# Kernel tuning notes

Hardware: AMD Instinct MI355X
Metric: run time of the kernel (lower is better)

Reference implementation:

```python
import jax, jax.numpy as jnp
import numpy as np

NUM_HEADS = 12

def setup_inputs() -> dict:
    key = jax.random.key(0)
    k1, k2, k3 = jax.random.split(key, 3)
    B, N, C = 8, 1024, 768
    x = jax.random.normal(k1, (B, N, C), dtype=jnp.float32)
    w_qkv = jax.random.normal(k2, (3 * C, C), dtype=jnp.float32) * (C ** -0.5)
    w_proj = jax.random.normal(k3, (C, C), dtype=jnp.float32) * (C ** -0.5)
    b_proj = jnp.zeros((C,), dtype=jnp.float32)
    return {"x": x, "w_qkv": w_qkv, "w_proj": w_proj, "b_proj": b_proj}

def reference(x, w_qkv, w_proj, b_proj):
    B, N, C = x.shape
    H = NUM_HEADS
    D = C // H
    scale = D ** -0.5
    # qkv projection: [B, N, 3C] -> [3, B, H, N, D]
    qkv = (x @ w_qkv.T).reshape(B, N, 3, H, D).transpose(2, 0, 3, 1, 4)
    q, k, v = qkv[0], qkv[1], qkv[2]
    # full N x N attention scores (unfused, as in the original module)
    attn = jnp.einsum("bhnd,bhmd->bhnm", q, k) * scale
    attn = jax.nn.softmax(attn, axis=-1)
    # attn_drop is identity at eval (p=0.0)
    out = jnp.einsum("bhnm,bhmd->bhnd", attn, v)  # [B, H, N, D]
    out = out.transpose(0, 2, 1, 3).reshape(B, N, C)
    out = out @ w_proj.T + b_proj
    # proj_drop identity at eval
    return (out, attn)
```

## Files before the change

### kernel.cpp

```cpp
#include <hip/hip_runtime.h>

#define Bb 8
#define Nn 1024
#define Cc 768
#define Hh 12
#define Dd 64
#define BHn (Bb*Hh)
#define Mm (Bb*Nn)
#define TCc (3*Cc)

typedef __bf16 bf16x8 __attribute__((ext_vector_type(8)));
typedef float  f32x4  __attribute__((ext_vector_type(4)));
typedef __attribute__((address_space(1))) const void* gas_ptr;
typedef __attribute__((address_space(3))) void* las_ptr;
typedef unsigned short u16;

__device__ __forceinline__ u16 bf16_rne(float f) {
    unsigned int u = __builtin_bit_cast(unsigned int, f);
    u += 0x7fffu + ((u >> 16) & 1u);
    return (u16)(u >> 16);
}
__device__ __forceinline__ void split_bf16(float f, u16& h, u16& l) {
    u16 hh = bf16_rne(f);
    float hf = __builtin_bit_cast(float, (unsigned int)hh << 16);
    h = hh;
    l = bf16_rne(f - hf);
}

__global__ __launch_bounds__(256)
void split_kernel(const float* __restrict__ src, u16* __restrict__ dh,
                  u16* __restrict__ dl, int n4)
{
    int stride = gridDim.x * blockDim.x;
    for (int i = blockIdx.x * blockDim.x + threadIdx.x; i < n4; i += stride) {
        float4 v = reinterpret_cast<const float4*>(src)[i];
        ushort4 h, l;
        split_bf16(v.x, h.x, l.x);
        split_bf16(v.y, h.y, l.y);
        split_bf16(v.z, h.z, l.z);
        split_bf16(v.w, h.w, l.w);
        reinterpret_cast<ushort4*>(dh)[i] = h;
        reinterpret_cast<ushort4*>(dl)[i] = l;
    }
}

__device__ __forceinline__ void gemm128_bf16x3(
    const u16* __restrict__ Agh, const u16* __restrict__ Agl,
    const u16* __restrict__ Bgh, const u16* __restrict__ Bgl,
    int m0, int j0, f32x4 acc[4][4])
{
    __shared__ __align__(16) u16 Ash[128*32];
    __shared__ __align__(16) u16 Asl[128*32];
    __shared__ __align__(16) u16 Bsh[128*32];
    __shared__ __align__(16) u16 Bsl[128*32];

    const int tid = threadIdx.x;
    const int ln = tid & 63, wid = tid >> 6;
    const int wr = wid >> 1, wc = wid & 1;

    const u16* gsrc =
        (wid == 0) ? Agh + (size_t)m0 * Cc :
        (wid == 1) ? Agl + (size_t)m0 * Cc :
        (wid == 2) ? Bgh + (size_t)j0 * Cc :
                     Bgl + (size_t)j0 * Cc;
    u16* lds = (wid == 0) ? Ash : (wid == 1) ? Asl : (wid == 2) ? Bsh : Bsl;

    const int lrow = ln >> 2, lslot = ln & 3;
    const int r16 = ln & 15,  ko = ln >> 4;

    f32x4 z = {0.f, 0.f, 0.f, 0.f};
#pragma unroll
    for (int mi = 0; mi < 4; ++mi)
#pragma unroll
        for (int ni = 0; ni < 4; ++ni) acc[mi][ni] = z;

    for (int k0 = 0; k0 < Cc; k0 += 32) {
#pragma unroll
        for (int c = 0; c < 8; ++c) {
            int row = c * 16 + lrow;
            int ss = lslot ^ ((row >> 1) & 3);
            const u16* gp = gsrc + (size_t)row * Cc + k0 + ss * 8;
            __builtin_amdgcn_global_load_lds((gas_ptr)gp, (las_ptr)(lds + c * 512), 16u, 0, 0);
        }
        __syncthreads();

        bf16x8 ah[4], al[4], bh[4], bl[4];
#pragma unroll
        for (int mi = 0; mi < 4; ++mi) {
            int row = wr*64 + mi*16 + r16;
            int ss = (ko ^ ((row >> 1) & 3)) * 8;
            ah[mi] = *reinterpret_cast<const bf16x8*>(Ash + row*32 + ss);
            al[mi] = *reinterpret_cast<const bf16x8*>(Asl + row*32 + ss);
        }
#pragma unroll
        for (int ni = 0; ni < 4; ++ni) {
            int row = wc*64 + ni*16 + r16;
            int ss = (ko ^ ((row >> 1) & 3)) * 8;
            bh[ni] = *reinterpret_cast<const bf16x8*>(Bsh + row*32 + ss);
            bl[ni] = *reinterpret_cast<const bf16x8*>(Bsl + row*32 + ss);
        }
#pragma unroll
        for (int mi = 0; mi < 4; ++mi)
#pragma unroll
            for (int ni = 0; ni < 4; ++ni) {
                acc[mi][ni] = __builtin_amdgcn_mfma_f32_16x16x32_bf16(ah[mi], bh[ni], acc[mi][ni], 0, 0, 0);
                acc[mi][ni] = __builtin_amdgcn_mfma_f32_16x16x32_bf16(ah[mi], bl[ni], acc[mi][ni], 0, 0, 0);
                acc[mi][ni] = __builtin_amdgcn_mfma_f32_16x16x32_bf16(al[mi], bh[ni], acc[mi][ni], 0, 0, 0);
            }
        __syncthreads();
    }
}

__global__ __launch_bounds__(256, 2)
void qkv_mfma(const u16* __restrict__ xh, const u16* __restrict__ xl,
              const u16* __restrict__ wh, const u16* __restrict__ wl,
              u16* __restrict__ Qh, u16* __restrict__ Ql,
              u16* __restrict__ Kh, u16* __restrict__ Kl,
              u16* __restrict__ Vth, u16* __restrict__ Vtl)
{
    const int m0 = blockIdx.x * 128, j0 = blockIdx.y * 128;
    f32x4 acc[4][4];
    gemm128_bf16x3(xh, xl, wh, wl, m0, j0, acc);

    const int tid = threadIdx.x;
    const int ln = tid & 63, wid = tid >> 6;
    const int wr = wid >> 1, wc = wid & 1;
    const int t3 = j0 / Cc;
    const int jr0 = j0 - t3 * Cc;

    if (t3 == 2) {
#pragma unroll
        for (int mi = 0; mi < 4; ++mi) {
            int gm0 = m0 + wr*64 + mi*16 + (ln >> 4) * 4;
            int b = gm0 >> 10, n0 = gm0 & 1023;
#pragma unroll
            for (int ni = 0; ni < 4; ++ni) {
                int col = jr0 + wc*64 + ni*16 + (ln & 15);
                int h = col >> 6, d = col & 63;
                u16 hh[4], ll[4];
#pragma unroll
                for (int i = 0; i < 4; ++i) split_bf16(acc[mi][ni][i], hh[i], ll[i]);
                size_t base = ((size_t)((b*Hh + h) * Dd + d)) * Nn + n0;
                *reinterpret_cast<ushort4*>(Vth + base) = make_ushort4(hh[0], hh[1], hh[2], hh[3]);
                *reinterpret_cast<ushort4*>(Vtl + base) = make_ushort4(ll[0], ll[1], ll[2], ll[3]);
            }
        }
    } else {
        u16* dh = (t3 == 0) ? Qh : Kh;
        u16* dl = (t3 == 0) ? Ql : Kl;
#pragma unroll
        for (int mi = 0; mi < 4; ++mi) {
            int gm0 = m0 + wr*64 + mi*16 + (ln >> 4) * 4;
            int b = gm0 >> 10, n0 = gm0 & 1023;
#pragma unroll
            for (int ni = 0; ni < 4; ++ni) {
                int col = jr0 + wc*64 + ni*16 + (ln & 15);
                int h = col >> 6, d = col & 63;
#pragma unroll
                for (int i = 0; i < 4; ++i) {
                    u16 hh, ll;
                    split_bf16(acc[mi][ni][i], hh, ll);
                    size_t base = ((size_t)((b*Hh + h) * Nn + n0 + i)) * Dd + d;
                    dh[base] = hh; dl[base] = ll;
                }
            }
        }
    }
}

__global__ __launch_bounds__(256, 2)
void scores_mfma(const u16* __restrict__ Qh_, const u16* __restrict__ Ql_,
                 const u16* __restrict__ Kh_, const u16* __restrict__ Kl_,
                 float* __restrict__ E, float* __restrict__ rowsum)
{
    __shared__ __align__(16) u16 sQh[128*64];
    __shared__ __align__(16) u16 sQl[128*64];
    __shared__ __align__(16) u16 sKh[128*64];
    __shared__ __align__(16) u16 sKl[128*64];

    const int tid = threadIdx.x;
    const int ln = tid & 63, wid = tid >> 6;
    const int wr = wid >> 1, wc = wid & 1;
    const int bh = blockIdx.z;
    const int i0 = blockIdx.x * 128, j0 = blockIdx.y * 128;
    const int r16 = ln & 15, ko = ln >> 4;

    {
        const u16* gsrc =
            (wid == 0) ? Qh_ + (size_t)(bh*Nn + i0) * Dd :
            (wid == 1) ? Ql_ + (size_t)(bh*Nn + i0) * Dd :
            (wid == 2) ? Kh_ + (size_t)(bh*Nn + j0) * Dd :
                         Kl_ + (size_t)(bh*Nn + j0) * Dd;
        u16* lds = (wid == 0) ? sQh : (wid == 1) ? sQl : (wid == 2) ? sKh : sKl;
        int r = ln >> 3, s = ln & 7;
        int ss = s ^ (r & 7);
        const u16* gp = gsrc + r*64 + ss*8;
#pragma unroll
        for (int c = 0; c < 16; ++c)
            __builtin_amdgcn_global_load_lds((gas_ptr)(gp + c*512), (las_ptr)(lds + c*512), 16u, 0, 0);
    }
    __syncthreads();

    f32x4 acc[4][4];
    f32x4 z = {0.f, 0.f, 0.f, 0.f};
#pragma unroll
    for (int mi = 0; mi < 4; ++mi)
#pragma unroll
        for (int ni = 0; ni < 4; ++ni) acc[mi][ni] = z;

#pragma unroll
    for (int kk = 0; kk < 2; ++kk) {
        bf16x8 qh[4], ql[4], kh[4], kl[4];
#pragma unroll
        for (int mi = 0; mi < 4; ++mi) {
            int row = wr*64 + mi*16 + r16;
            int s = (kk*4 + ko) ^ (row & 7);
            qh[mi] = *reinterpret_cast<const bf16x8*>(sQh + row*64 + s*8);
            ql[mi] = *reinterpret_cast<const bf16x8*>(sQl + row*64 + s*8);
        }
#pragma unroll
        for (int ni = 0; ni < 4; ++ni) {
            int row = wc*64 + ni*16 + r16;
            int s = (kk*4 + ko) ^ (row & 7);
            kh[ni] = *reinterpret_cast<const bf16x8*>(sKh + row*64 + s*8);
            kl[ni] = *reinterpret_cast<const bf16x8*>(sKl + row*64 + s*8);
        }
#pragma unroll
        for (int mi = 0; mi < 4; ++mi)
#pragma unroll
            for (int ni = 0; ni < 4; ++ni) {
                acc[mi][ni] = __builtin_amdgcn_mfma_f32_16x16x32_bf16(qh[mi], kh[ni], acc[mi][ni], 0, 0, 0);
                acc[mi][ni] = __builtin_amdgcn_mfma_f32_16x16x32_bf16(qh[mi], kl[ni], acc[mi][ni], 0, 0, 0);
                acc[mi][ni] = __builtin_amdgcn_mfma_f32_16x16x32_bf16(ql[mi], kh[ni], acc[mi][ni], 0, 0, 0);
            }
    }

    const float scale = 0.125f;
    float* Eb = E + (size_t)bh * Nn * Nn;
    float vsum[4][4];
#pragma unroll
    for (int mi = 0; mi < 4; ++mi)
#pragma unroll
        for (int i = 0; i < 4; ++i) vsum[mi][i] = 0.f;

#pragma unroll
    for (int mi = 0; mi < 4; ++mi) {
        int row = i0 + wr*64 + mi*16 + ko*4;
#pragma unroll
        for (int ni = 0; ni < 4; ++ni) {
            int col = j0 + wc*64 + ni*16 + r16;
#pragma unroll
            for (int i = 0; i < 4; ++i) {
                float v = __expf(acc[mi][ni][i] * scale);
                vsum[mi][i] += v;
                Eb[(size_t)(row + i) * Nn + col] = v;
            }
        }
    }
#pragma unroll
    for (int mi = 0; mi < 4; ++mi)
#pragma unroll
        for (int i = 0; i < 4; ++i) {
            float v = vsum[mi][i];
            v += __shfl_xor(v, 1); v += __shfl_xor(v, 2);
            v += __shfl_xor(v, 4); v += __shfl_xor(v, 8);
            vsum[mi][i] = v;
        }
    {
        int mi = r16 >> 2, i = r16 & 3;
        int row = i0 + wr*64 + mi*16 + ko*4 + i;
        atomicAdd(&rowsum[bh * Nn + row], vsum[mi][i]);
    }
}

__global__ __launch_bounds__(256, 2)
void pv_mfma(float* __restrict__ E, const u16* __restrict__ Vth, const u16* __restrict__ Vtl,
             const float* __restrict__ rowsum,
             u16* __restrict__ Oh, u16* __restrict__ Ol)
{
    __shared__ __align__(16) u16 sPh[128*64];
    __shared__ __align__(16) u16 sPl[128*64];
    __shared__ __align__(16) u16 sVh[64*64];
    __shared__ __align__(16) u16 sVl[64*64];
    __shared__ float inv_s[128];

    const int tid = threadIdx.x;
    const int ln = tid & 63, wid = tid >> 6;
    const int i0 = blockIdx.x * 128;
    const int bh = blockIdx.y;
    const int r16 = ln & 15, ko = ln >> 4;
    float* Eb = E + (size_t)bh * Nn * Nn;

    if (tid < 128) inv_s[tid] = 1.0f / rowsum[bh * Nn + i0 + tid];
    __syncthreads();

    f32x4 acc[2][4];
    f32x4 z = {0.f, 0.f, 0.f, 0.f};
#pragma unroll
    for (int mi = 0; mi < 2; ++mi)
#pragma unroll
        for (int ni = 0; ni < 4; ++ni) acc[mi][ni] = z;

    for (int j0 = 0; j0 < Nn; j0 += 64) {
        if (wid < 2) {
            const u16* gsrc = ((wid == 0) ? Vth : Vtl) + (size_t)bh * Dd * Nn + j0;
            u16* lds = (wid == 0) ? sVh : sVl;
            int r = ln >> 3, s = ln & 7;
            int ss = s ^ (r & 7);
            const u16* gp = gsrc + (size_t)r * Nn + ss*8;
#pragma unroll
            for (int c = 0; c < 8; ++c)
                __builtin_amdgcn_global_load_lds((gas_ptr)(gp + (size_t)c*8*Nn), (las_ptr)(lds + c*512), 16u, 0, 0);
        }
#pragma unroll
        for (int it = 0; it < 8; ++it) {
            int idx = tid + it * 256;
            int row = idx >> 4, c4 = idx & 15;
            float* gp = Eb + (size_t)(i0 + row) * Nn + j0 + c4*4;
            float4 e = *reinterpret_cast<const float4*>(gp);
            float is = inv_s[row];
            float4 p = make_float4(e.x*is, e.y*is, e.z*is, e.w*is);
            *reinterpret_cast<float4*>(gp) = p;
            u16 h[4], l[4];
            split_bf16(p.x, h[0], l[0]); split_bf16(p.y, h[1], l[1]);
            split_bf16(p.z, h[2], l[2]); split_bf16(p.w, h[3], l[3]);
            int s = (c4 >> 1) ^ (row & 7);
            int off = row*64 + s*8 + (c4 & 1)*4;
            *reinterpret_cast<ushort4*>(sPh + off) = make_ushort4(h[0], h[1], h[2], h[3]);
            *reinterpret_cast<ushort4*>(sPl + off) = make_ushort4(l[0], l[1], l[2], l[3]);
        }
        __syncthreads();

#pragma unroll
        for (int kk = 0; kk < 2; ++kk) {
            bf16x8 ph[2], pl[2], vh[4], vl[4];
#pragma unroll
            for (int mi = 0; mi < 2; ++mi) {
                int row = wid*32 + mi*16 + r16;
                int s = (kk*4 + ko) ^ (row & 7);
                ph[mi] = *reinterpret_cast<const bf16x8*>(sPh + row*64 + s*8);
                pl[mi] = *reinterpret_cast<const bf16x8*>(sPl + row*64 + s*8);
            }
#pragma unroll
            for (int ni = 0; ni < 4; ++ni) {
                int row = ni*16 + r16;
                int s = (kk*4 + ko) ^ (row & 7);
                vh[ni] = *reinterpret_cast<const bf16x8*>(sVh + row*64 + s*8);
                vl[ni] = *reinterpret_cast<const bf16x8*>(sVl + row*64 + s*8);
            }
#pragma unroll
            for (int mi = 0; mi < 2; ++mi)
#pragma unroll
                for (int ni = 0; ni < 4; ++ni) {
                    acc[mi][ni] = __builtin_amdgcn_mfma_f32_16x16x32_bf16(ph[mi], vh[ni], acc[mi][ni], 0, 0, 0);
                    acc[mi][ni] = __builtin_amdgcn_mfma_f32_16x16x32_bf16(ph[mi], vl[ni], acc[mi][ni], 0, 0, 0);
                    acc[mi][ni] = __builtin_amdgcn_mfma_f32_16x16x32_bf16(pl[mi], vh[ni], acc[mi][ni], 0, 0, 0);
                }
        }
        __syncthreads();
    }

    const int b = bh / Hh, h = bh % Hh;
#pragma unroll
    for (int mi = 0; mi < 2; ++mi) {
        int n0 = i0 + wid*32 + mi*16 + ko*4;
#pragma unroll
        for (int ni = 0; ni < 4; ++ni) {
            int d = ni*16 + r16;
#pragma unroll
            for (int i = 0; i < 4; ++i) {
                u16 hh, ll;
                split_bf16(acc[mi][ni][i], hh, ll);
                size_t base = ((size_t)(b * Nn + n0 + i)) * Cc + h * Dd + d;
                Oh[base] = hh; Ol[base] = ll;
            }
        }
    }
}

__global__ __launch_bounds__(256, 2)
void proj_mfma(const u16* __restrict__ oh, const u16* __restrict__ ol,
               const u16* __restrict__ wh, const u16* __restrict__ wl,
               const float* __restrict__ bias, float* __restrict__ out)
{
    const int m0 = blockIdx.x * 128, j0 = blockIdx.y * 128;
    f32x4 acc[4][4];
    gemm128_bf16x3(oh, ol, wh, wl, m0, j0, acc);

    const int tid = threadIdx.x;
    const int ln = tid & 63, wid = tid >> 6;
    const int wr = wid >> 1, wc = wid & 1;
#pragma unroll
    for (int mi = 0; mi < 4; ++mi) {
        int gm0 = m0 + wr*64 + mi*16 + (ln >> 4) * 4;
#pragma unroll
        for (int ni = 0; ni < 4; ++ni) {
            int col = j0 + wc*64 + ni*16 + (ln & 15);
            float bv = bias[col];
#pragma unroll
            for (int i = 0; i < 4; ++i)
                out[(size_t)(gm0 + i) * Cc + col] = acc[mi][ni][i] + bv;
        }
    }
}

extern "C" void kernel_launch(void* const* d_in, const int* in_sizes, int n_in,
                              void* d_out, int out_size, void* d_ws, size_t ws_size,
                              hipStream_t stream)
{
    const float* x      = (const float*)d_in[0];
    const float* w_qkv  = (const float*)d_in[1];
    const float* w_proj = (const float*)d_in[2];
    const float* b_proj = (const float*)d_in[3];

    float* out  = (float*)d_out;
    float* attn = out + (size_t)Mm * Cc;

    const size_t qkv_elems = (size_t)BHn * Nn * Dd;
    u16* Qh  = (u16*)d_ws;
    u16* Ql  = Qh  + qkv_elems;
    u16* Kh  = Ql  + qkv_elems;
    u16* Kl  = Kh  + qkv_elems;
    u16* Vth = Kl  + qkv_elems;
    u16* Vtl = Vth + qkv_elems;
    float* Oslot  = (float*)(Vtl + qkv_elems);
    float* rowsum = Oslot + (size_t)Mm * Cc;
    u16* wph = (u16*)(rowsum + (size_t)BHn * Nn);
    u16* wpl = wph + (size_t)Cc * Cc;

    u16* Oh = (u16*)Oslot;
    u16* Ol = Oh + (size_t)Mm * Cc;

    u16* xh  = (u16*)attn;
    u16* xl  = xh + (size_t)Mm * Cc;
    u16* wqh = xl + (size_t)Mm * Cc;
    u16* wql = wqh + (size_t)TCc * Cc;

    hipMemsetAsync(rowsum, 0, (size_t)BHn * Nn * sizeof(float), stream);

    split_kernel<<<dim3(2048), 256, 0, stream>>>(x,      xh,  xl,  (int)((size_t)Mm * Cc / 4));
    split_kernel<<<dim3(1728), 256, 0, stream>>>(w_qkv,  wqh, wql, (int)((size_t)TCc * Cc / 4));
    split_kernel<<<dim3(576),  256, 0, stream>>>(w_proj, wph, wpl, (int)((size_t)Cc * Cc / 4));

    qkv_mfma   <<<dim3(Mm/128, TCc/128), 256, 0, stream>>>(xh, xl, wqh, wql,
                                                           Qh, Ql, Kh, Kl, Vth, Vtl);
    scores_mfma<<<dim3(Nn/128, Nn/128, BHn), 256, 0, stream>>>(Qh, Ql, Kh, Kl, attn, rowsum);
    pv_mfma    <<<dim3(Nn/128, BHn), 256, 0, stream>>>(attn, Vth, Vtl, rowsum, Oh, Ol);
    proj_mfma  <<<dim3(Mm/128, Cc/128), 256, 0, stream>>>(Oh, Ol, wph, wpl, b_proj, out);
}
```

Before: 855.9 us.

## Fuse scores and PV into two-pass attention kernel with pre-swizzled Q/K layout

Replaces the separate scores and PV kernels with one fused attention kernel. A first pass recomputes QK^T to accumulate row sums of exp. A second pass recomputes the scores, writes normalized probabilities once, and feeds them straight into the PV MFMAs. This removes the unnormalized score write plus the read-modify-write of the full attention matrix, along with the atomic rowsum and the memset. In exchange, QK^T is computed twice. The QKV GEMM epilogue now stages Q/K through LDS and writes them in an XOR-swizzled tile image, so the fused kernel can load them with contiguous direct-to-LDS loads. Blocks are also remapped for locality.

```diff
diff --git a/kernel.cpp b/kernel.cpp
--- a/kernel.cpp
+++ b/kernel.cpp
@@ -25,6 +25,10 @@
     float hf = __builtin_bit_cast(float, (unsigned int)hh << 16);
     h = hh;
     l = bf16_rne(f - hf);
+}
+
+__device__ __forceinline__ int img_off(int row, int d) {
+    return row*64 + (((d >> 3) ^ (row & 7)) << 3) + (d & 7);
 }
 
 __global__ __launch_bounds__(256)
@@ -118,6 +122,7 @@
               u16* __restrict__ Kh, u16* __restrict__ Kl,
               u16* __restrict__ Vth, u16* __restrict__ Vtl)
 {
+    __shared__ __align__(16) u16 Rs[16384];
     const int m0 = blockIdx.x * 128, j0 = blockIdx.y * 128;
     f32x4 acc[4][4];
     gemm128_bf16x3(xh, xl, wh, wl, m0, j0, acc);
@@ -125,17 +130,20 @@
     const int tid = threadIdx.x;
     const int ln = tid & 63, wid = tid >> 6;
     const int wr = wid >> 1, wc = wid & 1;
+    const int r16 = ln & 15, ko = ln >> 4;
     const int t3 = j0 / Cc;
     const int jr0 = j0 - t3 * Cc;
+    const int b = m0 >> 10, nt = (m0 >> 7) & 7;
+    const int h1 = jr0 >> 6;
 
     if (t3 == 2) {
 #pragma unroll
         for (int mi = 0; mi < 4; ++mi) {
-            int gm0 = m0 + wr*64 + mi*16 + (ln >> 4) * 4;
-            int b = gm0 >> 10, n0 = gm0 & 1023;
-#pragma unroll
-            for (int ni = 0; ni < 4; ++ni) {
-                int col = jr0 + wc*64 + ni*16 + (ln & 15);
+            int gm0 = m0 + wr*64 + mi*16 + ko*4;
+            int n0 = gm0 & 1023;
+#pragma unroll
+            for (int ni = 0; ni < 4; ++ni) {
+                int col = jr0 + wc*64 + ni*16 + r16;
                 int h = col >> 6, d = col & 63;
                 u16 hh[4], ll[4];
 #pragma unroll
@@ -149,186 +157,222 @@
         u16* dh = (t3 == 0) ? Qh : Kh;
         u16* dl = (t3 == 0) ? Ql : Kl;
 #pragma unroll
-        for (int mi = 0; mi < 4; ++mi) {
-            int gm0 = m0 + wr*64 + mi*16 + (ln >> 4) * 4;
-            int b = gm0 >> 10, n0 = gm0 & 1023;
-#pragma unroll
-            for (int ni = 0; ni < 4; ++ni) {
-                int col = jr0 + wc*64 + ni*16 + (ln & 15);
-                int h = col >> 6, d = col & 63;
-#pragma unroll
-                for (int i = 0; i < 4; ++i) {
-                    u16 hh, ll;
-                    split_bf16(acc[mi][ni][i], hh, ll);
-                    size_t base = ((size_t)((b*Hh + h) * Nn + n0 + i)) * Dd + d;
-                    dh[base] = hh; dl[base] = ll;
+        for (int pass = 0; pass < 2; ++pass) {
+#pragma unroll
+            for (int mi = 0; mi < 4; ++mi)
+#pragma unroll
+                for (int ni = 0; ni < 4; ++ni)
+#pragma unroll
+                    for (int i = 0; i < 4; ++i) {
+                        int row = wr*64 + mi*16 + ko*4 + i;
+                        int col = wc*64 + ni*16 + r16;
+                        float v = acc[mi][ni][i];
+                        u16 hh = bf16_rne(v);
+                        u16 val = hh;
+                        if (pass) {
+                            float hf = __builtin_bit_cast(float, (unsigned int)hh << 16);
+                            val = bf16_rne(v - hf);
+                        }
+                        Rs[(col >> 6) * 8192 + img_off(row, col & 63)] = val;
+                    }
+            __syncthreads();
+            u16* gout = pass ? dl : dh;
+#pragma unroll
+            for (int it = 0; it < 8; ++it) {
+                int off = (it * 256 + tid) * 8;
+                int hd = off >> 13, w16 = off & 8191;
+                u16* gp = gout + ((size_t)((b*Hh + h1 + hd) * 8 + nt)) * 8192 + w16;
+                *reinterpret_cast<uint4*>(gp) = *reinterpret_cast<const uint4*>(&Rs[off]);
+            }
+            __syncthreads();
+        }
+    }
+}
+
+__global__ __launch_bounds__(256, 2)
+void attn_fused(const u16* __restrict__ Qh_, const u16* __restrict__ Ql_,
+                const u16* __restrict__ Kh_, const u16* __restrict__ Kl_,
+                const u16* __restrict__ Vth, const u16* __restrict__ Vtl,
+                float* __restrict__ E, u16* __restrict__ Oh, u16* __restrict__ Ol)
+{
+    __shared__ __align__(16) u16 pool[32768];
+    u16* sKh = pool;
+    u16* sKl = pool + 4096;
+    u16* sVh = pool + 8192;
+    u16* sVl = pool + 12288;
+    u16* sPh = pool + 16384;
+    u16* sPl = pool + 24576;
+    u16* sQh = pool + 16384;
+    u16* sQl = pool + 24576;
+
+    const int tid = threadIdx.x;
+    const int ln = tid & 63, w = tid >> 6;
+    const int r16 = ln & 15, ko = ln >> 4;
+
+    const int lid = blockIdx.x;
+    const int swz = (lid & 7) * 96 + (lid >> 3);
+    const int i0 = (swz & 7) * 128;
+    const int bh = swz >> 3;
+
+    {
+        const size_t qbase = ((size_t)bh * 8 + (i0 >> 7)) * 8192;
+        const u16* src = ((w < 2) ? Qh_ : Ql_) + qbase;
+        u16* dst = (w < 2) ? sQh : sQl;
+        int cbase = (w & 1) * 8;
+#pragma unroll
+        for (int c = 0; c < 8; ++c)
+            __builtin_amdgcn_global_load_lds((gas_ptr)(src + (cbase + c) * 512 + ln * 8),
+                                             (las_ptr)(dst + (cbase + c) * 512), 16u, 0, 0);
+    }
+    __syncthreads();
+    bf16x8 qh[2][2], ql[2][2];
+#pragma unroll
+    for (int mi = 0; mi < 2; ++mi) {
+        int row = w*32 + mi*16 + r16;
+#pragma unroll
+        for (int kk = 0; kk < 2; ++kk) {
+            int idx = row*64 + ((kk*4 + ko) ^ (row & 7)) * 8;
+            qh[mi][kk] = *reinterpret_cast<const bf16x8*>(sQh + idx);
+            ql[mi][kk] = *reinterpret_cast<const bf16x8*>(sQl + idx);
+        }
+    }
+    __syncthreads();
+
+    const float scale = 0.125f;
+    const f32x4 z = {0.f, 0.f, 0.f, 0.f};
+
+    float vsum[2][4];
+#pragma unroll
+    for (int mi = 0; mi < 2; ++mi)
+#pragma unroll
+        for (int i = 0; i < 4; ++i) vsum[mi][i] = 0.f;
+
+    for (int j0 = 0; j0 < Nn; j0 += 64) {
+        const size_t kbase = ((size_t)bh * 8 + (j0 >> 7)) * 8192 + ((j0 >> 6) & 1) * 4096;
+        {
+            const u16* src = ((w >> 1) ? Kl_ : Kh_) + kbase;
+            u16* dst = (w >> 1) ? sKl : sKh;
+            int cbase = (w & 1) * 4;
+#pragma unroll
+            for (int c = 0; c < 4; ++c)
+                __builtin_amdgcn_global_load_lds((gas_ptr)(src + (cbase + c) * 512 + ln * 8),
+                                                 (las_ptr)(dst + (cbase + c) * 512), 16u, 0, 0);
+        }
+        __syncthreads();
+
+        f32x4 acc[2][4];
+#pragma unroll
+        for (int mi = 0; mi < 2; ++mi)
+#pragma unroll
+            for (int ni = 0; ni < 4; ++ni) acc[mi][ni] = z;
+#pragma unroll
+        for (int kk = 0; kk < 2; ++kk) {
+            bf16x8 kh[4], kl[4];
+#pragma unroll
+            for (int ni = 0; ni < 4; ++ni) {
+                int row = ni*16 + r16;
+                int idx = row*64 + ((kk*4 + ko) ^ (row & 7)) * 8;
+                kh[ni] = *reinterpret_cast<const bf16x8*>(sKh + idx);
+                kl[ni] = *reinterpret_cast<const bf16x8*>(sKl + idx);
+            }
+#pragma unroll
+            for (int mi = 0; mi < 2; ++mi)
+#pragma unroll
+                for (int ni = 0; ni < 4; ++ni) {
+                    acc[mi][ni] = __builtin_amdgcn_mfma_f32_16x16x32_bf16(qh[mi][kk], kh[ni], acc[mi][ni], 0, 0, 0);
+                    acc[mi][ni] = __builtin_amdgcn_mfma_f32_16x16x32_bf16(qh[mi][kk], kl[ni], acc[mi][ni], 0, 0, 0);
+                    acc[mi][ni] = __builtin_amdgcn_mfma_f32_16x16x32_bf16(ql[mi][kk], kh[ni], acc[mi][ni], 0, 0, 0);
                 }
-            }
-        }
-    }
-}
-
-__global__ __launch_bounds__(256, 2)
-void scores_mfma(const u16* __restrict__ Qh_, const u16* __restrict__ Ql_,
-                 const u16* __restrict__ Kh_, const u16* __restrict__ Kl_,
-                 float* __restrict__ E, float* __restrict__ rowsum)
-{
-    __shared__ __align__(16) u16 sQh[128*64];
-    __shared__ __align__(16) u16 sQl[128*64];
-    __shared__ __align__(16) u16 sKh[128*64];
-    __shared__ __align__(16) u16 sKl[128*64];
-
-    const int tid = threadIdx.x;
-    const int ln = tid & 63, wid = tid >> 6;
-    const int wr = wid >> 1, wc = wid & 1;
-    const int bh = blockIdx.z;
-    const int i0 = blockIdx.x * 128, j0 = blockIdx.y * 128;
-    const int r16 = ln & 15, ko = ln >> 4;
-
-    {
-        const u16* gsrc =
-            (wid == 0) ? Qh_ + (size_t)(bh*Nn + i0) * Dd :
-            (wid == 1) ? Ql_ + (size_t)(bh*Nn + i0) * Dd :
-            (wid == 2) ? Kh_ + (size_t)(bh*Nn + j0) * Dd :
-                         Kl_ + (size_t)(bh*Nn + j0) * Dd;
-        u16* lds = (wid == 0) ? sQh : (wid == 1) ? sQl : (wid == 2) ? sKh : sKl;
-        int r = ln >> 3, s = ln & 7;
-        int ss = s ^ (r & 7);
-        const u16* gp = gsrc + r*64 + ss*8;
-#pragma unroll
-        for (int c = 0; c < 16; ++c)
-            __builtin_amdgcn_global_load_lds((gas_ptr)(gp + c*512), (las_ptr)(lds + c*512), 16u, 0, 0);
-    }
-    __syncthreads();
-
-    f32x4 acc[4][4];
-    f32x4 z = {0.f, 0.f, 0.f, 0.f};
-#pragma unroll
-    for (int mi = 0; mi < 4; ++mi)
-#pragma unroll
-        for (int ni = 0; ni < 4; ++ni) acc[mi][ni] = z;
-
-#pragma unroll
-    for (int kk = 0; kk < 2; ++kk) {
-        bf16x8 qh[4], ql[4], kh[4], kl[4];
-#pragma unroll
-        for (int mi = 0; mi < 4; ++mi) {
-            int row = wr*64 + mi*16 + r16;
-            int s = (kk*4 + ko) ^ (row & 7);
-            qh[mi] = *reinterpret_cast<const bf16x8*>(sQh + row*64 + s*8);
-            ql[mi] = *reinterpret_cast<const bf16x8*>(sQl + row*64 + s*8);
-        }
-#pragma unroll
-        for (int ni = 0; ni < 4; ++ni) {
-            int row = wc*64 + ni*16 + r16;
-            int s = (kk*4 + ko) ^ (row & 7);
-            kh[ni] = *reinterpret_cast<const bf16x8*>(sKh + row*64 + s*8);
-            kl[ni] = *reinterpret_cast<const bf16x8*>(sKl + row*64 + s*8);
-        }
-#pragma unroll
-        for (int mi = 0; mi < 4; ++mi)
-#pragma unroll
-            for (int ni = 0; ni < 4; ++ni) {
-                acc[mi][ni] = __builtin_amdgcn_mfma_f32_16x16x32_bf16(qh[mi], kh[ni], acc[mi][ni], 0, 0, 0);
-                acc[mi][ni] = __builtin_amdgcn_mfma_f32_16x16x32_bf16(qh[mi], kl[ni], acc[mi][ni], 0, 0, 0);
-                acc[mi][ni] = __builtin_amdgcn_mfma_f32_16x16x32_bf16(ql[mi], kh[ni], acc[mi][ni], 0, 0, 0);
-            }
-    }
-
-    const float scale = 0.125f;
-    float* Eb = E + (size_t)bh * Nn * Nn;
-    float vsum[4][4];
-#pragma unroll
-    for (int mi = 0; mi < 4; ++mi)
-#pragma unroll
-        for (int i = 0; i < 4; ++i) vsum[mi][i] = 0.f;
-
-#pragma unroll
-    for (int mi = 0; mi < 4; ++mi) {
-        int row = i0 + wr*64 + mi*16 + ko*4;
-#pragma unroll
-        for (int ni = 0; ni < 4; ++ni) {
-            int col = j0 + wc*64 + ni*16 + r16;
-#pragma unroll
-            for (int i = 0; i < 4; ++i) {
-                float v = __expf(acc[mi][ni][i] * scale);
-                vsum[mi][i] += v;
-                Eb[(size_t)(row + i) * Nn + col] = v;
-            }
-        }
-    }
-#pragma unroll
-    for (int mi = 0; mi < 4; ++mi)
+        }
+        __syncthreads();
+#pragma unroll
+        for (int mi = 0; mi < 2; ++mi)
+#pragma unroll
+            for (int ni = 0; ni < 4; ++ni)
+#pragma unroll
+                for (int i = 0; i < 4; ++i)
+                    vsum[mi][i] += __expf(acc[mi][ni][i] * scale);
+    }
+
+    float inv[2][4];
+#pragma unroll
+    for (int mi = 0; mi < 2; ++mi)
 #pragma unroll
         for (int i = 0; i < 4; ++i) {
             float v = vsum[mi][i];
             v += __shfl_xor(v, 1); v += __shfl_xor(v, 2);
             v += __shfl_xor(v, 4); v += __shfl_xor(v, 8);
-            vsum[mi][i] = v;
-        }
-    {
-        int mi = r16 >> 2, i = r16 & 3;
-        int row = i0 + wr*64 + mi*16 + ko*4 + i;
-        atomicAdd(&rowsum[bh * Nn + row], vsum[mi][i]);
-    }
-}
-
-__global__ __launch_bounds__(256, 2)
-void pv_mfma(float* __restrict__ E, const u16* __restrict__ Vth, const u16* __restrict__ Vtl,
-             const float* __restrict__ rowsum,
-             u16* __restrict__ Oh, u16* __restrict__ Ol)
-{
-    __shared__ __align__(16) u16 sPh[128*64];
-    __shared__ __align__(16) u16 sPl[128*64];
-    __shared__ __align__(16) u16 sVh[64*64];
-    __shared__ __align__(16) u16 sVl[64*64];
-    __shared__ float inv_s[128];
-
-    const int tid = threadIdx.x;
-    const int ln = tid & 63, wid = tid >> 6;
-    const int i0 = blockIdx.x * 128;
-    const int bh = blockIdx.y;
-    const int r16 = ln & 15, ko = ln >> 4;
+            inv[mi][i] = 1.0f / v;
+        }
+
+    f32x4 oacc[2][4];
+#pragma unroll
+    for (int mi = 0; mi < 2; ++mi)
+#pragma unroll
+        for (int ni = 0; ni < 4; ++ni) oacc[mi][ni] = z;
     float* Eb = E + (size_t)bh * Nn * Nn;
 
-    if (tid < 128) inv_s[tid] = 1.0f / rowsum[bh * Nn + i0 + tid];
-    __syncthreads();
-
-    f32x4 acc[2][4];
-    f32x4 z = {0.f, 0.f, 0.f, 0.f};
-#pragma unroll
-    for (int mi = 0; mi < 2; ++mi)
-#pragma unroll
-        for (int ni = 0; ni < 4; ++ni) acc[mi][ni] = z;
-
     for (int j0 = 0; j0 < Nn; j0 += 64) {
-        if (wid < 2) {
-            const u16* gsrc = ((wid == 0) ? Vth : Vtl) + (size_t)bh * Dd * Nn + j0;
-            u16* lds = (wid == 0) ? sVh : sVl;
-            int r = ln >> 3, s = ln & 7;
-            int ss = s ^ (r & 7);
-            const u16* gp = gsrc + (size_t)r * Nn + ss*8;
+        const size_t kbase = ((size_t)bh * 8 + (j0 >> 7)) * 8192 + ((j0 >> 6) & 1) * 4096;
+        if (w < 2) {
+            const u16* src = (w ? Kl_ : Kh_) + kbase;
+            u16* dst = w ? sKl : sKh;
 #pragma unroll
             for (int c = 0; c < 8; ++c)
-                __builtin_amdgcn_global_load_lds((gas_ptr)(gp + (size_t)c*8*Nn), (las_ptr)(lds + c*512), 16u, 0, 0);
-        }
-#pragma unroll
-        for (int it = 0; it < 8; ++it) {
-            int idx = tid + it * 256;
-            int row = idx >> 4, c4 = idx & 15;
-            float* gp = Eb + (size_t)(i0 + row) * Nn + j0 + c4*4;
-            float4 e = *reinterpret_cast<const float4*>(gp);
-            float is = inv_s[row];
-            float4 p = make_float4(e.x*is, e.y*is, e.z*is, e.w*is);
-            *reinterpret_cast<float4*>(gp) = p;
-            u16 h[4], l[4];
-            split_bf16(p.x, h[0], l[0]); split_bf16(p.y, h[1], l[1]);
-            split_bf16(p.z, h[2], l[2]); split_bf16(p.w, h[3], l[3]);
-            int s = (c4 >> 1) ^ (row & 7);
-            int off = row*64 + s*8 + (c4 & 1)*4;
-            *reinterpret_cast<ushort4*>(sPh + off) = make_ushort4(h[0], h[1], h[2], h[3]);
-            *reinterpret_cast<ushort4*>(sPl + off) = make_ushort4(l[0], l[1], l[2], l[3]);
-        }
+                __builtin_amdgcn_global_load_lds((gas_ptr)(src + c * 512 + ln * 8),
+                                                 (las_ptr)(dst + c * 512), 16u, 0, 0);
+        } else {
+            const u16* src0 = ((w == 2) ? Vth : Vtl) + (size_t)bh * Dd * Nn + j0;
+            u16* dst = (w == 2) ? sVh : sVl;
+            int r = ln >> 3, s = ln & 7, ss = s ^ (r & 7);
+            const u16* gp = src0 + (size_t)r * Nn + ss * 8;
+#pragma unroll
+            for (int c = 0; c < 8; ++c)
+                __builtin_amdgcn_global_load_lds((gas_ptr)(gp + (size_t)c * 8 * Nn),
+                                                 (las_ptr)(dst + c * 512), 16u, 0, 0);
+        }
+        __syncthreads();
+
+        f32x4 acc[2][4];
+#pragma unroll
+        for (int mi = 0; mi < 2; ++mi)
+#pragma unroll
+            for (int ni = 0; ni < 4; ++ni) acc[mi][ni] = z;
+#pragma unroll
+        for (int kk = 0; kk < 2; ++kk) {
+            bf16x8 kh[4], kl[4];
+#pragma unroll
+            for (int ni = 0; ni < 4; ++ni) {
+                int row = ni*16 + r16;
+                int idx = row*64 + ((kk*4 + ko) ^ (row & 7)) * 8;
+                kh[ni] = *reinterpret_cast<const bf16x8*>(sKh + idx);
+                kl[ni] = *reinterpret_cast<const bf16x8*>(sKl + idx);
+            }
+#pragma unroll
+            for (int mi = 0; mi < 2; ++mi)
+#pragma unroll
+                for (int ni = 0; ni < 4; ++ni) {
+                    acc[mi][ni] = __builtin_amdgcn_mfma_f32_16x16x32_bf16(qh[mi][kk], kh[ni], acc[mi][ni], 0, 0, 0);
+                    acc[mi][ni] = __builtin_amdgcn_mfma_f32_16x16x32_bf16(qh[mi][kk], kl[ni], acc[mi][ni], 0, 0, 0);
+                    acc[mi][ni] = __builtin_amdgcn_mfma_f32_16x16x32_bf16(ql[mi][kk], kh[ni], acc[mi][ni], 0, 0, 0);
+                }
+        }
+
+#pragma unroll
+        for (int mi = 0; mi < 2; ++mi)
+#pragma unroll
+            for (int ni = 0; ni < 4; ++ni) {
+                int colL = ni*16 + r16;
+#pragma unroll
+                for (int i = 0; i < 4; ++i) {
+                    int rowL = w*32 + mi*16 + ko*4 + i;
+                    float p = __expf(acc[mi][ni][i] * scale) * inv[mi][i];
+                    Eb[(size_t)(i0 + rowL) * Nn + j0 + colL] = p;
+                    u16 hh, ll; split_bf16(p, hh, ll);
+                    int idx = img_off(rowL, colL);
+                    sPh[idx] = hh; sPl[idx] = ll;
+                }
+            }
         __syncthreads();
 
 #pragma unroll
@@ -336,25 +380,25 @@
             bf16x8 ph[2], pl[2], vh[4], vl[4];
 #pragma unroll
             for (int mi = 0; mi < 2; ++mi) {
-                int row = wid*32 + mi*16 + r16;
-                int s = (kk*4 + ko) ^ (row & 7);
-                ph[mi] = *reinterpret_cast<const bf16x8*>(sPh + row*64 + s*8);
-                pl[mi] = *reinterpret_cast<const bf16x8*>(sPl + row*64 + s*8);
+                int row = w*32 + mi*16 + r16;
+                int idx = row*64 + ((kk*4 + ko) ^ (row & 7)) * 8;
+                ph[mi] = *reinterpret_cast<const bf16x8*>(sPh + idx);
+                pl[mi] = *reinterpret_cast<const bf16x8*>(sPl + idx);
             }
 #pragma unroll
             for (int ni = 0; ni < 4; ++ni) {
                 int row = ni*16 + r16;
-                int s = (kk*4 + ko) ^ (row & 7);
-                vh[ni] = *reinterpret_cast<const bf16x8*>(sVh + row*64 + s*8);
-                vl[ni] = *reinterpret_cast<const bf16x8*>(sVl + row*64 + s*8);
+                int idx = row*64 + ((kk*4 + ko) ^ (row & 7)) * 8;
+                vh[ni] = *reinterpret_cast<const bf16x8*>(sVh + idx);
+                vl[ni] = *reinterpret_cast<const bf16x8*>(sVl + idx);
             }
 #pragma unroll
             for (int mi = 0; mi < 2; ++mi)
 #pragma unroll
                 for (int ni = 0; ni < 4; ++ni) {
-                    acc[mi][ni] = __builtin_amdgcn_mfma_f32_16x16x32_bf16(ph[mi], vh[ni], acc[mi][ni], 0, 0, 0);
-                    acc[mi][ni] = __builtin_amdgcn_mfma_f32_16x16x32_bf16(ph[mi], vl[ni], acc[mi][ni], 0, 0, 0);
-                    acc[mi][ni] = __builtin_amdgcn_mfma_f32_16x16x32_bf16(pl[mi], vh[ni], acc[mi][ni], 0, 0, 0);
+                    oacc[mi][ni] = __builtin_amdgcn_mfma_f32_16x16x32_bf16(ph[mi], vh[ni], oacc[mi][ni], 0, 0, 0);
+                    oacc[mi][ni] = __builtin_amdgcn_mfma_f32_16x16x32_bf16(ph[mi], vl[ni], oacc[mi][ni], 0, 0, 0);
+                    oacc[mi][ni] = __builtin_amdgcn_mfma_f32_16x16x32_bf16(pl[mi], vh[ni], oacc[mi][ni], 0, 0, 0);
                 }
         }
         __syncthreads();
@@ -362,20 +406,18 @@
 
     const int b = bh / Hh, h = bh % Hh;
 #pragma unroll
-    for (int mi = 0; mi < 2; ++mi) {
-        int n0 = i0 + wid*32 + mi*16 + ko*4;
+    for (int mi = 0; mi < 2; ++mi)
 #pragma unroll
         for (int ni = 0; ni < 4; ++ni) {
             int d = ni*16 + r16;
 #pragma unroll
             for (int i = 0; i < 4; ++i) {
-                u16 hh, ll;
-                split_bf16(acc[mi][ni][i], hh, ll);
-                size_t base = ((size_t)(b * Nn + n0 + i)) * Cc + h * Dd + d;
+                int n = i0 + w*32 + mi*16 + ko*4 + i;
+                u16 hh, ll; split_bf16(oacc[mi][ni][i], hh, ll);
+                size_t base = ((size_t)(b * Nn + n)) * Cc + h * Dd + d;
                 Oh[base] = hh; Ol[base] = ll;
             }
         }
-    }
 }
 
 __global__ __launch_bounds__(256, 2)
@@ -424,8 +466,8 @@
     u16* Vth = Kl  + qkv_elems;
     u16* Vtl = Vth + qkv_elems;
     float* Oslot  = (float*)(Vtl + qkv_elems);
-    float* rowsum = Oslot + (size_t)Mm * Cc;
-    u16* wph = (u16*)(rowsum + (size_t)BHn * Nn);
+    float* gap    = Oslot + (size_t)Mm * Cc;
+    u16* wph = (u16*)(gap + (size_t)BHn * Nn);
     u16* wpl = wph + (size_t)Cc * Cc;
 
     u16* Oh = (u16*)Oslot;
@@ -436,15 +478,12 @@
     u16* wqh = xl + (size_t)Mm * Cc;
     u16* wql = wqh + (size_t)TCc * Cc;
 
-    hipMemsetAsync(rowsum, 0, (size_t)BHn * Nn * sizeof(float), stream);
-
     split_kernel<<<dim3(2048), 256, 0, stream>>>(x,      xh,  xl,  (int)((size_t)Mm * Cc / 4));
     split_kernel<<<dim3(1728), 256, 0, stream>>>(w_qkv,  wqh, wql, (int)((size_t)TCc * Cc / 4));
     split_kernel<<<dim3(576),  256, 0, stream>>>(w_proj, wph, wpl, (int)((size_t)Cc * Cc / 4));
 
-    qkv_mfma   <<<dim3(Mm/128, TCc/128), 256, 0, stream>>>(xh, xl, wqh, wql,
-                                                           Qh, Ql, Kh, Kl, Vth, Vtl);
-    scores_mfma<<<dim3(Nn/128, Nn/128, BHn), 256, 0, stream>>>(Qh, Ql, Kh, Kl, attn, rowsum);
-    pv_mfma    <<<dim3(Nn/128, BHn), 256, 0, stream>>>(attn, Vth, Vtl, rowsum, Oh, Ol);
-    proj_mfma  <<<dim3(Mm/128, Cc/128), 256, 0, stream>>>(Oh, Ol, wph, wpl, b_proj, out);
-}
+    qkv_mfma  <<<dim3(Mm/128, TCc/128), 256, 0, stream>>>(xh, xl, wqh, wql,
+                                                          Qh, Ql, Kh, Kl, Vth, Vtl);
+    attn_fused<<<dim3(768), 256, 0, stream>>>(Qh, Ql, Kh, Kl, Vth, Vtl, attn, Oh, Ol);
+    proj_mfma <<<dim3(Mm/128, Cc/128), 256, 0, stream>>>(Oh, Ol, wph, wpl, b_proj, out);
+}
```

Measured after the change: 708.7 us. -17.2%, faster.
